# Optimization experiments

Hardware: AMD Instinct MI355X
Metric: run time of the kernel (lower is better)

Reference implementation:

```python
import jax, jax.numpy as jnp
import numpy as np

B, N, C_IN, C_COORD, K = 2, 8192, 64, 3, 16
C_CAT = C_IN + C_COORD  # 67
HID1, HID2, C_OUT = 32, 64, 64


def setup_inputs() -> dict:
    key = jax.random.key(0)
    ks = jax.random.split(key, 10)
    s = 0.05
    return {
        "point_features": jax.random.normal(ks[0], (B, N, C_IN), jnp.float32),
        "coords": jax.random.uniform(ks[1], (B, N, C_COORD), jnp.float32),
        "w1": jax.random.normal(ks[2], (HID1, C_CAT), jnp.float32) * s,
        "b1": jax.random.normal(ks[3], (HID1,), jnp.float32) * s,
        "w2": jax.random.normal(ks[4], (HID2, HID1), jnp.float32) * s,
        "b2": jax.random.normal(ks[5], (HID2,), jnp.float32) * s,
        "w3": jax.random.normal(ks[6], (C_OUT, HID2), jnp.float32) * s,
        "b3": jax.random.normal(ks[7], (C_OUT,), jnp.float32) * s,
        "aggr_w": jax.random.normal(ks[8], (K,), jnp.float32) * s,
        "aggr_b": jax.random.normal(ks[9], (1,), jnp.float32) * s,
    }


def _knn_idx(coords):
    # squared pairwise distances: [B, N, N]
    sq = jnp.sum(coords * coords, axis=-1)
    d2 = sq[:, :, None] + sq[:, None, :] - 2.0 * jnp.einsum("bnc,bmc->bnm", coords, coords)
    # k smallest distances -> top_k of negated; self (d=0) lands at slot 0
    _, idx = jax.lax.top_k(-d2, K)  # [B, N, K]
    return idx


def reference(point_features, coords, w1, b1, w2, b2, w3, b3, aggr_w, aggr_b):
    idx = _knn_idx(coords)  # [B, N, K] int32
    feats = jnp.concatenate([point_features, coords], axis=-1)  # [B, N, C_CAT]
    # gather neighbor features -> [B, N, K, C_CAT]
    g = jax.vmap(lambda f, i: f[i])(feats, idx)
    # relative coords w.r.t. neighbor 0 (self)
    rel = g[..., -C_COORD:] - g[:, :, 0:1, -C_COORD:]
    g = jnp.concatenate([g[..., :C_IN], rel], axis=-1)
    # point pooling: max over K of raw input-feature channels
    y_pool = jnp.max(g[..., :C_IN], axis=2)  # [B, N, C_IN]
    # kernel MLP: stacked 1x1 convs, NO activations (act_func=None in source)
    h = jnp.einsum("bnkc,oc->bnko", g, w1) + b1
    h = jnp.einsum("bnkc,oc->bnko", h, w2) + b2
    h = jnp.einsum("bnkc,oc->bnko", h, w3) + b3  # [B, N, K, C_OUT]
    # attentive aggregation: Conv2d(K, 1, 1) over the K axis
    y_aggr = jnp.einsum("bnko,k->bno", h, aggr_w) + aggr_b  # [B, N, C_OUT]
    out_sum = jnp.sum(h, axis=2)  # [B, N, C_OUT]
    # concat order matches torch: (sum, pool, aggr), then permute -> B x N x C'
    return jnp.concatenate([out_sum, y_pool, y_aggr], axis=-1)
```

## Files before the change

### kernel.cpp

```cpp
#include <hip/hip_runtime.h>
#include <stdint.h>


typedef unsigned short u16;
typedef unsigned int   u32;
typedef unsigned long long u64;

#define NPTS  8192
#define KNB   16
#define SCAP  128
#define QPW   8

__device__ __forceinline__ float bf2f(u16 u) {
    union { u32 i; float f; } v; v.i = ((u32)u) << 16; return v.f;
}
__device__ __forceinline__ u16 f2bf(float f) {
    u32 x = __float_as_uint(f);
    return (u16)((x + 0x7FFFu + ((x >> 16) & 1u)) >> 16);
}
__device__ __forceinline__ u32 fordkey(float f) {
    u32 u = __float_as_uint(f);
    return u ^ ((u32)((int)u >> 31) | 0x80000000u);
}
__device__ __forceinline__ u64 shflxor64(u64 v, int m) {
    int lo = __shfl_xor((int)(u32)v, m, 64);
    int hi = __shfl_xor((int)(u32)(v >> 32), m, 64);
    return ((u64)(u32)hi << 32) | (u32)lo;
}
__device__ __forceinline__ float sq_np32(float x, float y, float z) {
    return __fadd_rn(__fadd_rn(__fmul_rn(x, x), __fmul_rn(y, y)), __fmul_rn(z, z));
}
__device__ __forceinline__ float d2_ref(float qx, float qy, float qz, float qsq,
                                        float x, float y, float z, float sq) {
    float dot = fmaf(z, qz, fmaf(y, qy, __fmul_rn(x, qx)));
    return __fsub_rn(__fadd_rn(qsq, sq), __fmul_rn(2.0f, dot));
}
__device__ __forceinline__ int cellof(float v) {
    int c = (int)floorf(v * 8.0f);
    return c < 0 ? 0 : (c > 7 ? 7 : c);
}

__global__ __launch_bounds__(256) void pack_count_kernel(
    const float* __restrict__ pf, const float* __restrict__ coords,
    u16* __restrict__ pfh, int* __restrict__ counts) {
    int gid = blockIdx.x * 256 + threadIdx.x;
    pfh[gid] = f2bf(pf[gid]);
    if (gid < 2 * NPTS) {
        float x = coords[gid * 3 + 0];
        float y = coords[gid * 3 + 1];
        float z = coords[gid * 3 + 2];
        int b = gid >> 13;
        int cell = (cellof(x) * 8 + cellof(y)) * 8 + cellof(z);
        atomicAdd(&counts[b * 512 + cell], 1);
    }
}

__global__ __launch_bounds__(512) void scan_kernel(
    const int* __restrict__ counts, int* __restrict__ cellStart,
    int* __restrict__ cellOffset) {
    __shared__ int s[512];
    int b = blockIdx.x, t = threadIdx.x;
    int myc = counts[b * 512 + t];
    s[t] = myc; __syncthreads();
#pragma unroll
    for (int off = 1; off < 512; off <<= 1) {
        int v = (t >= off) ? s[t - off] : 0; __syncthreads();
        s[t] += v; __syncthreads();
    }
    int excl = s[t] - myc;
    cellStart[b * 513 + t] = excl;
    cellOffset[b * 512 + t] = excl;
    if (t == 511) cellStart[b * 513 + 512] = s[511];
}

__global__ __launch_bounds__(256) void scatter_kernel(
    const float* __restrict__ coords, int* __restrict__ cellOffset,
    float4* __restrict__ spts, int* __restrict__ sidx) {
    int gid = blockIdx.x * 256 + threadIdx.x;
    float x = coords[gid * 3 + 0];
    float y = coords[gid * 3 + 1];
    float z = coords[gid * 3 + 2];
    int b = gid >> 13, i = gid & (NPTS - 1);
    int cell = (cellof(x) * 8 + cellof(y)) * 8 + cellof(z);
    int pos = atomicAdd(&cellOffset[b * 512 + cell], 1);
    spts[b * NPTS + pos] = make_float4(x, y, z, sq_np32(x, y, z));
    sidx[b * NPTS + pos] = i;
}

__global__ __launch_bounds__(64, 4) void knn_kernel(
    const float* __restrict__ coords, const float4* __restrict__ spts,
    const int* __restrict__ sidx, const int* __restrict__ cellStart,
    int* __restrict__ idx_out) {
    __shared__ u64 surv[SCAP];

    const int lane = threadIdx.x;
    const int blk  = blockIdx.x;
    const int b    = blk >> 11;
    const int q0   = (blk & 2047) * 4;
    const float*  cb = coords + (size_t)b * NPTS * 3;
    const float4* sp = spts + b * NPTS;
    const int*    si = sidx + b * NPTS;
    const int*    cs = cellStart + b * 513;

#pragma unroll 1
    for (int t = 0; t < 4; ++t) {
        const int q = q0 + t;
        float qx = cb[q * 3 + 0], qy = cb[q * 3 + 1], qz = cb[q * 3 + 2];
        float qsq = sq_np32(qx, qy, qz);
        int cqx = cellof(qx), cqy = cellof(qy), cqz = cellof(qz);

        int ax0 = max(cqx - 1, 0), ax1 = min(cqx + 1, 7);
        int ay0 = max(cqy - 1, 0), ay1 = min(cqy + 1, 7);
        int az0 = max(cqz - 1, 0), az1 = min(cqz + 1, 7);
        float dmin = 3.0e38f;
#pragma unroll 1
        for (int cx = ax0; cx <= ax1; ++cx)
#pragma unroll 1
            for (int cy = ay0; cy <= ay1; ++cy) {
                int base = (cx * 8 + cy) * 8;
                int s = cs[base + az0], e = cs[base + az1 + 1];
                for (int i0 = s; i0 < e; i0 += 64) {
                    int i = i0 + lane;
                    int ii = (i < e) ? i : (e - 1);
                    float4 c = sp[ii];
                    float d2 = d2_ref(qx, qy, qz, qsq, c.x, c.y, c.z, c.w);
                    if (i < e) dmin = fminf(dmin, d2);
                }
            }
        {
            float v = dmin;
#pragma unroll
            for (int k = 2; k <= 64; k <<= 1) {
#pragma unroll
                for (int j2 = k >> 1; j2 >= 1; j2 >>= 1) {
                    float o = __shfl_xor(v, j2, 64);
                    bool lo = (lane & j2) == 0;
                    bool up = (lane & k) == 0;
                    float mn = fminf(v, o), mx = fmaxf(v, o);
                    v = (lo == up) ? mn : mx;
                }
            }
            dmin = __shfl(v, 15, 64);
        }
        const float tau = dmin;

        float rr = sqrtf(tau + 1e-5f) + 1e-6f;
        int bx0 = max((int)floorf((qx - rr) * 8.0f), 0);
        int bx1 = min((int)floorf((qx + rr) * 8.0f), 7);
        int by0 = max((int)floorf((qy - rr) * 8.0f), 0);
        int by1 = min((int)floorf((qy + rr) * 8.0f), 7);
        int bz0 = max((int)floorf((qz - rr) * 8.0f), 0);
        int bz1 = min((int)floorf((qz + rr) * 8.0f), 7);
        int cnt = 0;
#pragma unroll 1
        for (int cx = bx0; cx <= bx1; ++cx)
#pragma unroll 1
            for (int cy = by0; cy <= by1; ++cy) {
                int base = (cx * 8 + cy) * 8;
                int s = cs[base + bz0], e = cs[base + bz1 + 1];
                for (int i0 = s; i0 < e; i0 += 64) {
                    int i = i0 + lane;
                    bool valid = (i < e);
                    int ii = valid ? i : (e - 1);
                    float4 c = sp[ii];
                    float d2 = d2_ref(qx, qy, qz, qsq, c.x, c.y, c.z, c.w);
                    bool pass = valid && (d2 <= tau);
                    u64 mask = __ballot(pass);
                    if (pass) {
                        int pre = __builtin_amdgcn_mbcnt_hi((u32)(mask >> 32),
                                  __builtin_amdgcn_mbcnt_lo((u32)mask, 0));
                        int pos = cnt + pre;
                        if (pos < SCAP)
                            surv[pos] = ((u64)fordkey(d2) << 32) | (u32)si[ii];
                    }
                    cnt += (int)__popcll(mask);
                }
            }
        __syncthreads();

        int myidx = 0;
        if (cnt <= 64) {
            u64 key = (lane < cnt) ? surv[lane] : ~0ull;
#pragma unroll
            for (int k = 2; k <= 64; k <<= 1) {
#pragma unroll
                for (int j2 = k >> 1; j2 >= 1; j2 >>= 1) {
                    u64 o = shflxor64(key, j2);
                    bool lo = (lane & j2) == 0;
                    bool up = (lane & k) == 0;
                    bool takemin = (lo == up);
                    key = ((o < key) == takemin) ? o : key;
                }
            }
            myidx = (int)(u32)(key & 0xffffffffu);
        } else {
            int cc = cnt > SCAP ? SCAP : cnt;
            u64 a0 = (lane < cc) ? surv[lane] : ~0ull;
            u64 a1 = (64 + lane < cc) ? surv[64 + lane] : ~0ull;
            if (a1 < a0) { u64 tmp = a0; a0 = a1; a1 = tmp; }
#pragma unroll 1
            for (int r = 0; r < 16; ++r) {
                u64 m = a0;
#pragma unroll
                for (int d = 1; d < 64; d <<= 1) {
                    u64 o = shflxor64(m, d);
                    m = (o < m) ? o : m;
                }
                if (a0 == m) { a0 = a1; a1 = ~0ull; }
                if (lane == r) myidx = (int)(u32)(m & 0xffffffffu);
            }
        }
        if (lane < KNB)
            idx_out[((size_t)b * NPTS + q) * KNB + lane] = myidx;
        __syncthreads();
    }
}

__global__ __launch_bounds__(64) void mlp_kernel(
    const u16* __restrict__ pfh, const float* __restrict__ coords,
    const float* __restrict__ w1, const float* __restrict__ b1,
    const float* __restrict__ w2, const float* __restrict__ b2,
    const float* __restrict__ w3, const float* __restrict__ b3,
    const float* __restrict__ aw, const float* __restrict__ ab,
    const int* __restrict__ knn_idx, const int* __restrict__ sidx,
    float* __restrict__ out) {

    __shared__ __attribute__((aligned(16))) float vbuf[2][68];
    __shared__ __attribute__((aligned(16))) float h1buf[2][36];

    const int lane = threadIdx.x;
    const int r    = lane & 31;
    const int vec  = lane >> 5;

    float w1r[68];
#pragma unroll
    for (int c = 0; c < 67; ++c) w1r[c] = w1[r * 67 + c];
    w1r[67] = 0.0f;
    float w2r[32];
    {
        const float4* p = (const float4*)(w2 + lane * 32);
#pragma unroll
        for (int c4 = 0; c4 < 8; ++c4) {
            float4 v = p[c4];
            w2r[c4 * 4 + 0] = v.x; w2r[c4 * 4 + 1] = v.y;
            w2r[c4 * 4 + 2] = v.z; w2r[c4 * 4 + 3] = v.w;
        }
    }
    float w3r[64];
    {
        const float4* p = (const float4*)(w3 + lane * 64);
#pragma unroll
        for (int c4 = 0; c4 < 16; ++c4) {
            float4 v = p[c4];
            w3r[c4 * 4 + 0] = v.x; w3r[c4 * 4 + 1] = v.y;
            w3r[c4 * 4 + 2] = v.z; w3r[c4 * 4 + 3] = v.w;
        }
    }
    float awr[16];
#pragma unroll
    for (int k = 0; k < 16; ++k) awr[k] = aw[k];
    float sa = 0.0f;
#pragma unroll
    for (int k = 0; k < 16; ++k) sa += awr[k];
    const float b1v = b1[r], b2v = b2[lane], b3v = b3[lane], abv = ab[0];
    const float c1 = (vec == 0) ? 16.0f : sa;

    const int sblk = (blockIdx.x & 7) * 256 + (blockIdx.x >> 3);

#pragma unroll 1
    for (int t = 0; t < QPW; ++t) {
        const int gp = sblk * QPW + t;
        const int b  = gp >> 13;
        const int q  = sidx[(size_t)b * NPTS + (gp & (NPTS - 1))];
        const int gq = b * NPTS + q;
        const u16*   pfb = pfh + (size_t)b * NPTS * 64;
        const float* cb  = coords + (size_t)b * NPTS * 3;

        int myi = knn_idx[(size_t)gq * KNB + (lane & 15)] & (NPTS - 1);

        float pool = -3.0e38f, G1 = 0.0f, Ga = 0.0f;
#pragma unroll
        for (int k = 0; k < 16; ++k) {
            int nk = __shfl(myi, k, 64);
            float v = bf2f(pfb[nk * 64 + lane]);
            pool = fmaxf(pool, v);
            G1 += v;
            Ga = fmaf(awr[k], v, Ga);
        }
        vbuf[0][lane] = G1;
        vbuf[1][lane] = Ga;

        if (lane < 48) {
            int j  = lane >> 4;
            int i0 = __shfl(myi, 0, 64);
            float rel  = cb[myi * 3 + j] - cb[i0 * 3 + j];
            float wrel = awr[lane & 15] * rel;
#pragma unroll
            for (int d = 1; d < 16; d <<= 1) {
                rel  += __shfl_xor(rel, d, 64);
                wrel += __shfl_xor(wrel, d, 64);
            }
            if ((lane & 15) == 0) { vbuf[0][64 + j] = rel; vbuf[1][64 + j] = wrel; }
        }
        if (lane == 0) { vbuf[0][67] = 0.0f; vbuf[1][67] = 0.0f; }
        __syncthreads();

        float acc = c1 * b1v;
        {
            const float4* vp = (const float4*)(&vbuf[vec][0]);
#pragma unroll
            for (int c4 = 0; c4 < 17; ++c4) {
                float4 g4 = vp[c4];
                acc = fmaf(g4.x, w1r[c4 * 4 + 0], acc);
                acc = fmaf(g4.y, w1r[c4 * 4 + 1], acc);
                acc = fmaf(g4.z, w1r[c4 * 4 + 2], acc);
                acc = fmaf(g4.w, w1r[c4 * 4 + 3], acc);
            }
        }
        h1buf[vec][r] = acc;
        __syncthreads();

        float a0 = 16.0f * b2v, a1 = sa * b2v;
        {
            const float4* p0 = (const float4*)(&h1buf[0][0]);
            const float4* p1 = (const float4*)(&h1buf[1][0]);
#pragma unroll
            for (int c4 = 0; c4 < 8; ++c4) {
                float4 x0 = p0[c4], x1 = p1[c4];
                a0 = fmaf(x0.x, w2r[c4 * 4 + 0], a0);
                a0 = fmaf(x0.y, w2r[c4 * 4 + 1], a0);
                a0 = fmaf(x0.z, w2r[c4 * 4 + 2], a0);
                a0 = fmaf(x0.w, w2r[c4 * 4 + 3], a0);
                a1 = fmaf(x1.x, w2r[c4 * 4 + 0], a1);
                a1 = fmaf(x1.y, w2r[c4 * 4 + 1], a1);
                a1 = fmaf(x1.z, w2r[c4 * 4 + 2], a1);
                a1 = fmaf(x1.w, w2r[c4 * 4 + 3], a1);
            }
        }
        __syncthreads();
        vbuf[0][lane] = a0;
        vbuf[1][lane] = a1;
        __syncthreads();

        float s1 = 16.0f * b3v, sA = sa * b3v;
        {
            const float4* p0 = (const float4*)(&vbuf[0][0]);
            const float4* p1 = (const float4*)(&vbuf[1][0]);
#pragma unroll
            for (int c4 = 0; c4 < 16; ++c4) {
                float4 x0 = p0[c4], x1 = p1[c4];
                s1 = fmaf(x0.x, w3r[c4 * 4 + 0], s1);
                s1 = fmaf(x0.y, w3r[c4 * 4 + 1], s1);
                s1 = fmaf(x0.z, w3r[c4 * 4 + 2], s1);
                s1 = fmaf(x0.w, w3r[c4 * 4 + 3], s1);
                sA = fmaf(x1.x, w3r[c4 * 4 + 0], sA);
                sA = fmaf(x1.y, w3r[c4 * 4 + 1], sA);
                sA = fmaf(x1.z, w3r[c4 * 4 + 2], sA);
                sA = fmaf(x1.w, w3r[c4 * 4 + 3], sA);
            }
        }
        float* op = out + (size_t)gq * 192;
        op[lane]       = s1;
        op[64 + lane]  = pool;
        op[128 + lane] = sA + abv;
        __syncthreads();
    }
}

extern "C" void kernel_launch(void* const* d_in, const int* in_sizes, int n_in,
                              void* d_out, int out_size, void* d_ws, size_t ws_size,
                              hipStream_t stream) {
    const float* pf     = (const float*)d_in[0];
    const float* coords = (const float*)d_in[1];
    const float* w1     = (const float*)d_in[2];
    const float* b1     = (const float*)d_in[3];
    const float* w2     = (const float*)d_in[4];
    const float* b2     = (const float*)d_in[5];
    const float* w3     = (const float*)d_in[6];
    const float* b3     = (const float*)d_in[7];
    const float* aw     = (const float*)d_in[8];
    const float* ab     = (const float*)d_in[9];

    char* ws = (char*)d_ws;
    int*    knn_idx    = (int*)ws;
    u16*    pfh        = (u16*)(ws + (1 << 20));
    float4* spts       = (float4*)(ws + (3 << 20));
    int*    sidx       = (int*)(ws + (3 << 20) + (256 << 10));
    int*    cellStart  = (int*)(ws + (3 << 20) + (320 << 10));
    int*    counts     = (int*)(ws + (3 << 20) + (328 << 10));
    int*    cellOffset = (int*)(ws + (3 << 20) + (336 << 10));
    float*  outp       = (float*)d_out;

    hipMemsetAsync(counts, 0, 2 * 512 * sizeof(int), stream);
    pack_count_kernel<<<4096, 256, 0, stream>>>(pf, coords, pfh, counts);
    scan_kernel<<<2, 512, 0, stream>>>(counts, cellStart, cellOffset);
    scatter_kernel<<<64, 256, 0, stream>>>(coords, cellOffset, spts, sidx);
    knn_kernel<<<4096, 64, 0, stream>>>(coords, spts, sidx, cellStart, knn_idx);
    mlp_kernel<<<2048, 64, 0, stream>>>(pfh, coords, w1, b1, w2, b2, w3, b3,
                                        aw, ab, knn_idx, sidx, outp);
}
```

Baseline: 152.3 us.

## Cache first-pass kNN distances in LDS and process queries in sorted cell order

The first-pass scan over the 3x3x3 neighbourhood now stores each candidate's distance key in a shared-memory buffer (up to 768 entries). The second pass filters that buffer against the threshold and only rescans cells outside the first neighbourhood. Queries are now taken from the cell-sorted point array, and blocks are interleaved across the grid, so queries near each other in space run together and global loads get better locality. Sorted indices are mapped back through sidx only at output time. The cost is extra LDS per block, which may lower occupancy, plus more branching and a fallback path when the buffer overflows.

```diff
diff --git a/kernel.cpp b/kernel.cpp
--- a/kernel.cpp
+++ b/kernel.cpp
@@ -9,6 +9,7 @@
 #define NPTS  8192
 #define KNB   16
 #define SCAP  128
+#define CAPA  768
 #define QPW   8
 
 __device__ __forceinline__ float bf2f(u16 u) {
@@ -87,32 +88,59 @@
     sidx[b * NPTS + pos] = i;
 }
 
+__device__ __forceinline__ void scan_seg(
+    const float4* __restrict__ sp, const int* __restrict__ cs,
+    u64* __restrict__ surv, int base, int z0, int z1,
+    float qx, float qy, float qz, float qsq, float tau, int lane, int& cnt) {
+    if (z0 > z1) return;
+    int s = cs[base + z0], e = cs[base + z1 + 1];
+    for (int i0 = s; i0 < e; i0 += 64) {
+        int i = i0 + lane;
+        bool valid = (i < e);
+        int ii = valid ? i : (e - 1);
+        float4 c = sp[ii];
+        float d2 = d2_ref(qx, qy, qz, qsq, c.x, c.y, c.z, c.w);
+        bool pass = valid && (d2 <= tau);
+        u64 mask = __ballot(pass);
+        if (pass) {
+            int pre = __builtin_amdgcn_mbcnt_hi((u32)(mask >> 32),
+                      __builtin_amdgcn_mbcnt_lo((u32)mask, 0));
+            int pos = cnt + pre;
+            if (pos < SCAP)
+                surv[pos] = ((u64)fordkey(d2) << 32) | (u32)ii;
+        }
+        cnt += (int)__popcll(mask);
+    }
+}
+
 __global__ __launch_bounds__(64, 4) void knn_kernel(
-    const float* __restrict__ coords, const float4* __restrict__ spts,
-    const int* __restrict__ sidx, const int* __restrict__ cellStart,
-    int* __restrict__ idx_out) {
+    const float4* __restrict__ spts, const int* __restrict__ sidx,
+    const int* __restrict__ cellStart, int* __restrict__ idx_out) {
+    __shared__ u64 allk[CAPA];
     __shared__ u64 surv[SCAP];
 
     const int lane = threadIdx.x;
     const int blk  = blockIdx.x;
-    const int b    = blk >> 11;
-    const int q0   = (blk & 2047) * 4;
-    const float*  cb = coords + (size_t)b * NPTS * 3;
+    const int sblk = (blk & 7) * 512 + (blk >> 3);
+    const int b    = sblk >> 11;
+    const int p0   = (sblk & 2047) * 4;
     const float4* sp = spts + b * NPTS;
     const int*    si = sidx + b * NPTS;
     const int*    cs = cellStart + b * 513;
 
 #pragma unroll 1
     for (int t = 0; t < 4; ++t) {
-        const int q = q0 + t;
-        float qx = cb[q * 3 + 0], qy = cb[q * 3 + 1], qz = cb[q * 3 + 2];
-        float qsq = sq_np32(qx, qy, qz);
+        const int p = p0 + t;
+        float4 qc = sp[p];
+        const float qx = qc.x, qy = qc.y, qz = qc.z, qsq = qc.w;
         int cqx = cellof(qx), cqy = cellof(qy), cqz = cellof(qz);
 
         int ax0 = max(cqx - 1, 0), ax1 = min(cqx + 1, 7);
         int ay0 = max(cqy - 1, 0), ay1 = min(cqy + 1, 7);
         int az0 = max(cqz - 1, 0), az1 = min(cqz + 1, 7);
         float dmin = 3.0e38f;
+        int cnt0 = 0;
+        bool ovf = false;
 #pragma unroll 1
         for (int cx = ax0; cx <= ax1; ++cx)
 #pragma unroll 1
@@ -121,12 +149,23 @@
                 int s = cs[base + az0], e = cs[base + az1 + 1];
                 for (int i0 = s; i0 < e; i0 += 64) {
                     int i = i0 + lane;
-                    int ii = (i < e) ? i : (e - 1);
+                    bool valid = (i < e);
+                    int ii = valid ? i : (e - 1);
                     float4 c = sp[ii];
                     float d2 = d2_ref(qx, qy, qz, qsq, c.x, c.y, c.z, c.w);
-                    if (i < e) dmin = fminf(dmin, d2);
-                }
-            }
+                    if (valid) dmin = fminf(dmin, d2);
+                    int add = (e - i0 < 64) ? (e - i0) : 64;
+                    if (!ovf && cnt0 + add <= CAPA) {
+                        if (valid)
+                            allk[cnt0 + lane] = ((u64)fordkey(d2) << 32) | (u32)ii;
+                        cnt0 += add;
+                    } else {
+                        ovf = true;
+                    }
+                }
+            }
+        __syncthreads();
+
         {
             float v = dmin;
 #pragma unroll
@@ -152,28 +191,38 @@
         int bz0 = max((int)floorf((qz - rr) * 8.0f), 0);
         int bz1 = min((int)floorf((qz + rr) * 8.0f), 7);
         int cnt = 0;
+        if (!ovf) {
+            const u32 taukey = fordkey(tau);
+            for (int i0 = 0; i0 < cnt0; i0 += 64) {
+                int i = i0 + lane;
+                bool valid = (i < cnt0);
+                u64 kk = valid ? allk[i] : ~0ull;
+                bool pass = valid && ((u32)(kk >> 32) <= taukey);
+                u64 mask = __ballot(pass);
+                if (pass) {
+                    int pre = __builtin_amdgcn_mbcnt_hi((u32)(mask >> 32),
+                              __builtin_amdgcn_mbcnt_lo((u32)mask, 0));
+                    int pos = cnt + pre;
+                    if (pos < SCAP) surv[pos] = kk;
+                }
+                cnt += (int)__popcll(mask);
+            }
+        }
 #pragma unroll 1
         for (int cx = bx0; cx <= bx1; ++cx)
 #pragma unroll 1
             for (int cy = by0; cy <= by1; ++cy) {
                 int base = (cx * 8 + cy) * 8;
-                int s = cs[base + bz0], e = cs[base + bz1 + 1];
-                for (int i0 = s; i0 < e; i0 += 64) {
-                    int i = i0 + lane;
-                    bool valid = (i < e);
-                    int ii = valid ? i : (e - 1);
-                    float4 c = sp[ii];
-                    float d2 = d2_ref(qx, qy, qz, qsq, c.x, c.y, c.z, c.w);
-                    bool pass = valid && (d2 <= tau);
-                    u64 mask = __ballot(pass);
-                    if (pass) {
-                        int pre = __builtin_amdgcn_mbcnt_hi((u32)(mask >> 32),
-                                  __builtin_amdgcn_mbcnt_lo((u32)mask, 0));
-                        int pos = cnt + pre;
-                        if (pos < SCAP)
-                            surv[pos] = ((u64)fordkey(d2) << 32) | (u32)si[ii];
-                    }
-                    cnt += (int)__popcll(mask);
+                bool colInA = !ovf && cx >= ax0 && cx <= ax1 &&
+                              cy >= ay0 && cy <= ay1;
+                if (colInA) {
+                    scan_seg(sp, cs, surv, base, bz0, min(az0 - 1, bz1),
+                             qx, qy, qz, qsq, tau, lane, cnt);
+                    scan_seg(sp, cs, surv, base, max(az1 + 1, bz0), bz1,
+                             qx, qy, qz, qsq, tau, lane, cnt);
+                } else {
+                    scan_seg(sp, cs, surv, base, bz0, bz1,
+                             qx, qy, qz, qsq, tau, lane, cnt);
                 }
             }
         __syncthreads();
@@ -210,8 +259,11 @@
                 if (lane == r) myidx = (int)(u32)(m & 0xffffffffu);
             }
         }
-        if (lane < KNB)
-            idx_out[((size_t)b * NPTS + q) * KNB + lane] = myidx;
+        if (lane < KNB) {
+            const int q = si[p];
+            idx_out[((size_t)b * NPTS + q) * KNB + lane] =
+                si[myidx & (NPTS - 1)];
+        }
         __syncthreads();
     }
 }
@@ -395,7 +447,7 @@
     pack_count_kernel<<<4096, 256, 0, stream>>>(pf, coords, pfh, counts);
     scan_kernel<<<2, 512, 0, stream>>>(counts, cellStart, cellOffset);
     scatter_kernel<<<64, 256, 0, stream>>>(coords, cellOffset, spts, sidx);
-    knn_kernel<<<4096, 64, 0, stream>>>(coords, spts, sidx, cellStart, knn_idx);
+    knn_kernel<<<4096, 64, 0, stream>>>(spts, sidx, cellStart, knn_idx);
     mlp_kernel<<<2048, 64, 0, stream>>>(pfh, coords, w1, b1, w2, b2, w3, b3,
                                         aw, ab, knn_idx, sidx, outp);
 }
```

Result: slower. 155.7 us (+2.2%).
